# Kernel tuning notes

Measured on AMD Instinct MI355X. Metric: run time of the kernel, lower is better.

Reference implementation:

```python
import math
import jax, jax.numpy as jnp
import numpy as np

B, IMG, CIN = 32, 32, 4
PATCH, HIDDEN, DEPTH, HEADS, MLP = 2, 768, 12, 12, 3072
FREQ, NUM_CLASSES = 256, 1000
GRID = IMG // PATCH
N = GRID * GRID
OUT = PATCH * PATCH * CIN


def _pos_embed(dim, length):
    # faithful port of get_2d_sincos_pos_embed
    g = int(math.sqrt(length))
    grid = np.stack(np.meshgrid(np.arange(g, dtype=np.float32),
                                np.arange(g, dtype=np.float32), indexing='ij')).reshape(2, -1)
    def emb1d(d, pos):
        omega = 1.0 / 10000.0 ** (np.arange(d // 2, dtype=np.float32) / (d / 2.0))
        out = np.einsum('m,d->md', pos, omega)
        return np.concatenate([np.sin(out), np.cos(out)], axis=1)
    pe = np.concatenate([emb1d(dim // 2, grid[0]), emb1d(dim // 2, grid[1])], axis=1)
    return jnp.asarray(pe[None], dtype=jnp.float32)  # [1, N, dim]


def _ln(x):
    # LayerNorm(elementwise_affine=False), eps=1e-5, biased variance
    m = jnp.mean(x, axis=-1, keepdims=True)
    v = jnp.var(x, axis=-1, keepdims=True)
    return (x - m) * jax.lax.rsqrt(v + 1e-5)


def setup_inputs() -> dict:
    key = jax.random.key(0)
    ks = jax.random.split(key, 20)
    w = lambda k, shape: jax.random.normal(k, shape, jnp.float32) * 0.02
    z = lambda *shape: jnp.zeros(shape, jnp.float32)
    return {
        'x': jax.random.normal(ks[0], (B, IMG, IMG, CIN), jnp.float32),
        't': jax.random.uniform(ks[1], (B,), jnp.float32) * 1000.0,
        'y': jax.random.randint(ks[2], (B,), 0, NUM_CLASSES + 1),
        'patch_w': w(ks[3], (PATCH * PATCH * CIN, HIDDEN)), 'patch_b': z(HIDDEN),
        't_w1': w(ks[4], (FREQ, HIDDEN)), 't_b1': z(HIDDEN),
        't_w2': w(ks[5], (HIDDEN, HIDDEN)), 't_b2': z(HIDDEN),
        'label_emb': w(ks[6], (NUM_CLASSES + 1, HIDDEN)),
        'ada_w': w(ks[7], (DEPTH, HIDDEN, 6 * HIDDEN)), 'ada_b': z(DEPTH, 6 * HIDDEN),
        'q_w': w(ks[8], (DEPTH, HIDDEN, HIDDEN)), 'q_b': z(DEPTH, HIDDEN),
        'k_w': w(ks[9], (DEPTH, HIDDEN, HIDDEN)), 'k_b': z(DEPTH, HIDDEN),
        'v_w': w(ks[10], (DEPTH, HIDDEN, HIDDEN)), 'v_b': z(DEPTH, HIDDEN),
        'o_w': w(ks[11], (DEPTH, HIDDEN, HIDDEN)), 'o_b': z(DEPTH, HIDDEN),
        'fc1_w': w(ks[12], (DEPTH, HIDDEN, MLP)), 'fc1_b': z(DEPTH, MLP),
        'fc2_w': w(ks[13], (DEPTH, MLP, HIDDEN)), 'fc2_b': z(DEPTH, HIDDEN),
        'fin_ada_w': w(ks[14], (HIDDEN, 2 * HIDDEN)), 'fin_ada_b': z(2 * HIDDEN),
        'fin_w': w(ks[15], (HIDDEN, OUT)), 'fin_b': z(OUT),
    }


def reference(x, t, y, patch_w, patch_b, t_w1, t_b1, t_w2, t_b2, label_emb,
              ada_w, ada_b, q_w, q_b, k_w, k_b, v_w, v_b, o_w, o_b,
              fc1_w, fc1_b, fc2_w, fc2_b, fin_ada_w, fin_ada_b, fin_w, fin_b):
    Bx = x.shape[0]
    dh = HIDDEN // HEADS
    # patch embed (conv k=p, stride=p == per-patch linear)
    patches = x.reshape(Bx, GRID, PATCH, GRID, PATCH, CIN)
    patches = patches.transpose(0, 1, 3, 2, 4, 5).reshape(Bx, N, PATCH * PATCH * CIN)
    h = patches @ patch_w + patch_b + _pos_embed(HIDDEN, N)
    # timestep embedding: [cos, sin] order
    half = FREQ // 2
    freqs = jnp.exp(-math.log(10000.0) * jnp.arange(half, dtype=jnp.float32) / half)
    args = t.astype(jnp.float32)[:, None] * freqs[None]
    temb = jnp.concatenate([jnp.cos(args), jnp.sin(args)], axis=-1)
    temb = jax.nn.silu(temb @ t_w1 + t_b1) @ t_w2 + t_b2
    c_act = jax.nn.silu(temb + label_emb[y])  # silu applied inside each block on c

    def block(hx, p):
        aw, ab, qw, qb, kw, kb, vw, vb, ow, ob, f1w, f1b, f2w, f2b = p
        ada = c_act @ aw + ab
        sh_m, sc_m, g_m, sh_p, sc_p, g_p = jnp.split(ada, 6, axis=-1)
        xn = _ln(hx) * (1.0 + sc_m[:, None]) + sh_m[:, None]
        q = ((xn @ qw + qb).reshape(Bx, N, HEADS, dh)) / math.sqrt(3.0)
        k = (xn @ kw + kb).reshape(Bx, N, HEADS, dh)
        v = (xn @ vw + vb).reshape(Bx, N, HEADS, dh)
        attn = jax.nn.softmax(jnp.einsum('bqhc,bkhc->bhqk', q, k).astype(jnp.float32), axis=-1)
        yv = jnp.einsum('bhqk,bkhc->bqhc', attn, v).reshape(Bx, N, HIDDEN)
        hx = hx + g_m[:, None] * (yv @ ow + ob)
        xn2 = _ln(hx) * (1.0 + sc_p[:, None]) + sh_p[:, None]
        mlp = jax.nn.gelu(xn2 @ f1w + f1b, approximate=False) @ f2w + f2b
        hx = hx + g_p[:, None] * mlp
        return hx, None

    h, _ = jax.lax.scan(block, h, (ada_w, ada_b, q_w, q_b, k_w, k_b, v_w, v_b,
                                   o_w, o_b, fc1_w, fc1_b, fc2_w, fc2_b))
    # final layer
    fada = c_act @ fin_ada_w + fin_ada_b
    sh, sc = jnp.split(fada, 2, axis=-1)
    out = (_ln(h) * (1.0 + sc[:, None]) + sh[:, None]) @ fin_w + fin_b
    return out  # [B, N, patch*patch*out_channels]
```

## Files before the change

kernel.cpp:

```cpp
#include <hip/hip_runtime.h>
#include <hip/hip_bf16.h>


typedef short  s16x8 __attribute__((ext_vector_type(8)));
typedef float  f32x4 __attribute__((ext_vector_type(4)));

__device__ __forceinline__ float bf2f(unsigned short u) {
    union { unsigned int i; float f; } v; v.i = ((unsigned int)u) << 16; return v.f;
}
__device__ __forceinline__ unsigned short f2bf(float f) {
    union { float f; unsigned int i; } v; v.f = f;
    unsigned int r = (v.i + 0x7FFFu + ((v.i >> 16) & 1u)) >> 16;
    return (unsigned short)r;
}
__device__ __forceinline__ float silu(float v) { return v / (1.f + __expf(-v)); }

__device__ __forceinline__ void gload16(const void* gptr, void* lptr) {
    __builtin_amdgcn_global_load_lds(
        (const __attribute__((address_space(1))) unsigned int*)gptr,
        (__attribute__((address_space(3))) unsigned int*)lptr,
        16, 0, 0);
}

#define ROWS 8192
#define HID  768
#define MLPD 3072
#define ADA_LD 4608

__global__ __launch_bounds__(256) void ada_init(const float* __restrict__ ada_b,
                                                const float* __restrict__ fada_b,
                                                const float* __restrict__ t_b1,
                                                const float* __restrict__ t_b2,
                                                const float* __restrict__ lemb,
                                                const int* __restrict__ y,
                                                float* __restrict__ ada_all,
                                                float* __restrict__ fada,
                                                float* __restrict__ z1,
                                                float* __restrict__ z2)
{
    const int bid = blockIdx.x, tid = threadIdx.x;
    if (bid >= 222) {
        const int col = (bid - 222) * 256 + tid;
        const float b1v = t_b1[col], b2v = t_b2[col];
        for (int r = 0; r < 32; ++r) {
            z1[(size_t)r * HID + col] = b1v;
            z2[(size_t)r * HID + col] = b2v + lemb[(size_t)y[r] * HID + col];
        }
        return;
    }
    const float* Bv; float* Out; int ldw, colb;
    if (bid < 216) {
        const int l = bid / 18; colb = (bid % 18) * 256;
        Bv = ada_b + (size_t)l * ADA_LD; Out = ada_all + (size_t)l * 32 * ADA_LD; ldw = ADA_LD;
    } else {
        colb = (bid - 216) * 256;
        Bv = fada_b; Out = fada; ldw = 1536;
    }
    const int col = colb + tid;
    const float bb = Bv[col];
    #pragma unroll
    for (int r = 0; r < 32; ++r) Out[(size_t)r * ldw + col] = bb;
}

__global__ __launch_bounds__(256) void temb1_k(const float* __restrict__ t,
                                               const float* __restrict__ w1,
                                               float* __restrict__ z1)
{
    __shared__ float tin[128];
    const int b = blockIdx.x, cc = blockIdx.y, kc = blockIdx.z, tid = threadIdx.x;
    const int k0 = kc * 128;
    if (tid < 128) {
        const int k = k0 + tid, j = k & 127;
        const float fr = __expf((float)j * (-9.210340371976184f / 128.f));
        const float a = t[b] * fr;
        tin[tid] = (k < 128) ? cosf(a) : sinf(a);
    }
    __syncthreads();
    const int col = cc * 256 + tid;
    float acc = 0.f;
    #pragma unroll 8
    for (int kk = 0; kk < 128; ++kk) acc += tin[kk] * w1[(size_t)(k0 + kk) * HID + col];
    atomicAdd(&z1[(size_t)b * HID + col], acc);
}

__global__ __launch_bounds__(256) void temb2_k(const float* __restrict__ z1,
                                               const float* __restrict__ w2,
                                               float* __restrict__ z2)
{
    __shared__ float tin[192];
    const int b = blockIdx.x, cc = blockIdx.y, kc = blockIdx.z, tid = threadIdx.x;
    const int k0 = kc * 192;
    if (tid < 192) tin[tid] = silu(z1[(size_t)b * HID + k0 + tid]);
    __syncthreads();
    const int col = cc * 256 + tid;
    float acc = 0.f;
    #pragma unroll 8
    for (int kk = 0; kk < 192; ++kk) acc += tin[kk] * w2[(size_t)(k0 + kk) * HID + col];
    atomicAdd(&z2[(size_t)b * HID + col], acc);
}

__global__ __launch_bounds__(64) void ada_gemm2(const float* __restrict__ z2,
                                                const float* __restrict__ ada_w,
                                                const float* __restrict__ fada_w,
                                                float* __restrict__ ada_all,
                                                float* __restrict__ fada)
{
    const int bx = blockIdx.x, kc = blockIdx.y, tid = threadIdx.x;
    const float* W; float* Out; int ldw, colb;
    if (bx < 216) {
        const int l = bx / 18; colb = (bx % 18) * 256;
        W = ada_w + (size_t)l * HID * ADA_LD; Out = ada_all + (size_t)l * 32 * ADA_LD; ldw = ADA_LD;
    } else {
        colb = (bx - 216) * 256;
        W = fada_w; Out = fada; ldw = 1536;
    }
    const int k0 = kc * 96;
    __shared__ float cs_[32][96];
    for (int i = tid; i < 32 * 96; i += 64)
        cs_[i / 96][i % 96] = silu(z2[(size_t)(i / 96) * HID + k0 + (i % 96)]);
    __syncthreads();
    float acc[4][32];
    #pragma unroll
    for (int j = 0; j < 4; ++j)
        #pragma unroll
        for (int r = 0; r < 32; ++r) acc[j][r] = 0.f;
    #pragma unroll 1
    for (int kk = 0; kk < 96; kk += 4) {
        float wv[4][4];
        #pragma unroll
        for (int i = 0; i < 4; ++i) {
            const float* Wr = W + (size_t)(k0 + kk + i) * ldw + colb + tid;
            #pragma unroll
            for (int j = 0; j < 4; ++j) wv[j][i] = Wr[64 * j];
        }
        #pragma unroll
        for (int r = 0; r < 32; ++r) {
            const float4 cv = *(const float4*)&cs_[r][kk];
            #pragma unroll
            for (int j = 0; j < 4; ++j)
                acc[j][r] += cv.x * wv[j][0] + cv.y * wv[j][1] + cv.z * wv[j][2] + cv.w * wv[j][3];
        }
    }
    #pragma unroll
    for (int j = 0; j < 4; ++j)
        #pragma unroll
        for (int r = 0; r < 32; ++r)
            atomicAdd(&Out[(size_t)r * ldw + colb + tid + 64 * j], acc[j][r]);
}

__global__ __launch_bounds__(256) void patch_embed(const float* __restrict__ x,
                                                   const float* __restrict__ pw,
                                                   const float* __restrict__ pb,
                                                   float* __restrict__ h)
{
    const int row = blockIdx.x;
    const int b = row >> 8, n = row & 255;
    const int gi = n >> 4, gj = n & 15;
    const int tid = threadIdx.x;
    __shared__ float pv[16];
    if (tid < 16) {
        const int pr = tid >> 3, pc = (tid >> 2) & 1, ci = tid & 3;
        pv[tid] = x[((size_t)(b * 32 + gi * 2 + pr) * 32 + (gj * 2 + pc)) * 4 + ci];
    }
    __syncthreads();
    #pragma unroll
    for (int cc = 0; cc < 3; ++cc) {
        const int col = cc * 256 + tid;
        float acc = pb[col];
        #pragma unroll
        for (int i = 0; i < 16; ++i) acc += pv[i] * pw[(size_t)i * HID + col];
        const int d4 = (col < 384) ? col : col - 384;
        const int pos = (col < 384) ? gi : gj;
        const float kf = (float)(d4 < 192 ? d4 : d4 - 192);
        const float om = __expf(kf * (-9.210340371976184f / 192.f));
        const float a = (float)pos * om;
        acc += (d4 < 192) ? sinf(a) : cosf(a);
        h[(size_t)row * HID + col] = acc;
    }
}

__global__ __launch_bounds__(256) void convert_weights(
    const float* __restrict__ q_w, const float* __restrict__ k_w,
    const float* __restrict__ v_w, const float* __restrict__ o_w,
    const float* __restrict__ fc1_w, const float* __restrict__ fc2_w,
    const float* __restrict__ q_b, const float* __restrict__ k_b,
    const float* __restrict__ v_b,
    unsigned short* __restrict__ wbase, size_t slot_stride,
    float* __restrict__ cbias, int first_layer)
{
    const int bid = blockIdx.x;
    const int l = first_layer + bid / 6913;
    const int t = bid % 6913;
    unsigned short* dst = wbase + (size_t)(bid / 6913) * slot_stride;
    const int tid = threadIdx.x;
    if (t == 6912) {
        float* cb = cbias + (size_t)l * 2304;
        for (int i = tid; i < 2304; i += 256) {
            float v;
            if (i < 768)       v = q_b[(size_t)l * 768 + i];
            else if (i < 1536) v = k_b[(size_t)l * 768 + i - 768];
            else               v = v_b[(size_t)l * 768 + i - 1536];
            cb[i] = v;
        }
        return;
    }
    const float* src; int srcN; unsigned short* d; int dLd; int tr, tc;
    if (t < 2304) {
        const int mat = t / 576, tt = t % 576; tr = tt / 24; tc = tt % 24;
        srcN = 768; dLd = 768;
        if (mat == 0)      { src = q_w + (size_t)l * 589824; d = dst; }
        else if (mat == 1) { src = k_w + (size_t)l * 589824; d = dst + 589824; }
        else if (mat == 2) { src = v_w + (size_t)l * 589824; d = dst + 1179648; }
        else               { src = o_w + (size_t)l * 589824; d = dst + 1769472; }
    } else if (t < 4608) {
        const int tt = t - 2304; tr = tt / 96; tc = tt % 96;
        src = fc1_w + (size_t)l * 2359296; srcN = 3072; dLd = 768; d = dst + 2359296;
    } else {
        const int tt = t - 4608; tr = tt / 24; tc = tt % 24;
        src = fc2_w + (size_t)l * 2359296; srcN = 768; dLd = 3072; d = dst + 4718592;
    }
    __shared__ float lt[32][33];
    const int tx = tid & 31, ty = tid >> 5;
    const int r0 = tr * 32, c0 = tc * 32;
    #pragma unroll
    for (int i = 0; i < 4; ++i)
        lt[ty + i * 8][tx] = src[(size_t)(r0 + ty + i * 8) * srcN + c0 + tx];
    __syncthreads();
    #pragma unroll
    for (int i = 0; i < 4; ++i)
        d[(size_t)(c0 + ty + i * 8) * dLd + r0 + tx] = f2bf(lt[tx][ty + i * 8]);
}

__global__ __launch_bounds__(192) void ln_mod(const float* __restrict__ hbuf,
                                              const float* __restrict__ mod,
                                              int sh_off, int sc_off, int mld,
                                              unsigned short* __restrict__ xout)
{
    const int row = blockIdx.x, tid = threadIdx.x;
    const float4 xv = *(const float4*)&hbuf[(size_t)row * HID + tid * 4];
    float s = (xv.x + xv.y) + (xv.z + xv.w);
    float ss = (xv.x * xv.x + xv.y * xv.y) + (xv.z * xv.z + xv.w * xv.w);
    #pragma unroll
    for (int d = 1; d < 64; d <<= 1) { s += __shfl_xor(s, d); ss += __shfl_xor(ss, d); }
    __shared__ float sb[3], ssb[3];
    if ((tid & 63) == 0) { sb[tid >> 6] = s; ssb[tid >> 6] = ss; }
    __syncthreads();
    s = sb[0] + sb[1] + sb[2];
    ss = ssb[0] + ssb[1] + ssb[2];
    const float mean = s * (1.f / 768.f);
    const float var = ss * (1.f / 768.f) - mean * mean;
    const float rs = rsqrtf(var + 1e-5f);
    const int b = row >> 8;
    const float* mrow = mod + (size_t)b * mld;
    const float4 sc = *(const float4*)&mrow[sc_off + tid * 4];
    const float4 sh = *(const float4*)&mrow[sh_off + tid * 4];
    ushort4 o;
    o.x = f2bf((xv.x - mean) * rs * (1.f + sc.x) + sh.x);
    o.y = f2bf((xv.y - mean) * rs * (1.f + sc.y) + sh.y);
    o.z = f2bf((xv.z - mean) * rs * (1.f + sc.z) + sh.z);
    o.w = f2bf((xv.w - mean) * rs * (1.f + sc.w) + sh.w);
    *(ushort4*)&xout[(size_t)row * HID + tid * 4] = o;
}

template<int EPI, int BN>
__global__ __launch_bounds__(256) void gemm_bt(const unsigned short* __restrict__ A,
                                               const unsigned short* __restrict__ Bt,
                                               const float* __restrict__ bias,
                                               void* __restrict__ outp,
                                               const float* __restrict__ gate,
                                               int K, int ldo)
{
    constexpr int BELEMS = BN * 32;
    constexpr int NJ = BN / 32;
    __shared__ unsigned short sAB[2][4096 + BELEMS];
    const int tid = threadIdx.x;
    const int lane = tid & 63;
    const int w = tid >> 6;
    const int wm = w >> 1, wn = w & 1;
    const int rowbase = blockIdx.y << 7;
    const int colbase = blockIdx.x * BN;
    const size_t a0 = (size_t)(rowbase +      (tid >> 2)) * K + (tid & 3) * 8;
    const size_t a1 = (size_t)(rowbase + 64 + (tid >> 2)) * K + (tid & 3) * 8;
    const size_t b0 = (size_t)(colbase +      (tid >> 2)) * K + (tid & 3) * 8;
    size_t b1 = 0;
    if constexpr (BN == 128)
        b1 = (size_t)(colbase + 64 + (tid >> 2)) * K + (tid & 3) * 8;
    const int ldsw = w * 512;
    f32x4 acc[4][NJ];
    #pragma unroll
    for (int i = 0; i < 4; ++i)
        #pragma unroll
        for (int j = 0; j < NJ; ++j) acc[i][j] = (f32x4){0.f, 0.f, 0.f, 0.f};
    const int nk = K >> 5;
    const int lm = lane & 15, lg = lane >> 4;
    {
        unsigned short* base = &sAB[0][0];
        gload16(A + a0,  base + ldsw);
        gload16(A + a1,  base + 2048 + ldsw);
        gload16(Bt + b0, base + 4096 + ldsw);
        if constexpr (BN == 128) gload16(Bt + b1, base + 6144 + ldsw);
    }
    __syncthreads();
    int cur = 0;
    for (int kt = 0; kt < nk; ++kt) {
        if (kt + 1 < nk) {
            const int k0 = (kt + 1) << 5;
            unsigned short* base = &sAB[cur ^ 1][0];
            gload16(A + a0 + k0,  base + ldsw);
            gload16(A + a1 + k0,  base + 2048 + ldsw);
            gload16(Bt + b0 + k0, base + 4096 + ldsw);
            if constexpr (BN == 128) gload16(Bt + b1 + k0, base + 6144 + ldsw);
        }
        const unsigned short* sAc = &sAB[cur][0];
        const unsigned short* sBc = &sAB[cur][4096];
        s16x8 af[4], bfr[NJ];
        #pragma unroll
        for (int mi = 0; mi < 4; ++mi)
            af[mi] = *(const s16x8*)&sAc[(wm * 64 + mi * 16 + lm) * 32 + lg * 8];
        #pragma unroll
        for (int nj = 0; nj < NJ; ++nj)
            bfr[nj] = *(const s16x8*)&sBc[(wn * (16 * NJ) + nj * 16 + lm) * 32 + lg * 8];
        #pragma unroll
        for (int mi = 0; mi < 4; ++mi)
            #pragma unroll
            for (int nj = 0; nj < NJ; ++nj)
                acc[mi][nj] = __builtin_amdgcn_mfma_f32_16x16x32_bf16(af[mi], bfr[nj], acc[mi][nj], 0, 0, 0);
        __syncthreads();
        cur ^= 1;
    }
    float bv[NJ], gv[NJ];
    #pragma unroll
    for (int nj = 0; nj < NJ; ++nj) {
        const int col = colbase + wn * (16 * NJ) + nj * 16 + lm;
        bv[nj] = bias[col];
        if constexpr (EPI == 2) gv[nj] = gate[(size_t)(rowbase >> 8) * ADA_LD + col];
    }
    #pragma unroll
    for (int mi = 0; mi < 4; ++mi) {
        const int row = rowbase + wm * 64 + mi * 16 + (lg << 2);
        #pragma unroll
        for (int nj = 0; nj < NJ; ++nj) {
            const int col = colbase + wn * (16 * NJ) + nj * 16 + lm;
            #pragma unroll
            for (int r = 0; r < 4; ++r) {
                const float v = acc[mi][nj][r] + bv[nj];
                if constexpr (EPI == 0) {
                    ((unsigned short*)outp)[(size_t)(row + r) * ldo + col] = f2bf(v);
                } else if constexpr (EPI == 1) {
                    const float g = 0.5f * v * (1.f + erff(v * 0.70710678118654752f));
                    ((unsigned short*)outp)[(size_t)(row + r) * ldo + col] = f2bf(g);
                } else {
                    float* O = (float*)outp;
                    const size_t idx = (size_t)(row + r) * ldo + col;
                    O[idx] = O[idx] + gv[nj] * v;
                }
            }
        }
    }
}

__global__ __launch_bounds__(256) void attn_fused(const unsigned short* __restrict__ qkv,
                                                  unsigned short* __restrict__ yv)
{
    __shared__ unsigned short Vt[64][264];
    __shared__ unsigned short Psm[4][32 * 72];
    __shared__ float Ssc[4][32];
    const int bid = blockIdx.x;
    const int b = bid / 24, rem = bid % 24, h = rem >> 1, half = rem & 1;
    const int tid = threadIdx.x, w = tid >> 6, lane = tid & 63;
    {
        const int dhg = tid & 7, tk = tid >> 3;
        #pragma unroll
        for (int g = 0; g < 8; ++g) {
            const int tok = tk + g * 32;
            s16x8 vv = *(const s16x8*)(qkv + (size_t)(b * 256 + tok) * 2304 + 1536 + h * 64 + dhg * 8);
            #pragma unroll
            for (int j = 0; j < 8; ++j) Vt[dhg * 8 + j][tok] = (unsigned short)vv[j];
        }
    }
    __syncthreads();
    const int q0 = half * 128 + w * 32;
    const int lm = lane & 15, lg = lane >> 4;
    const unsigned short* Qb = qkv + (size_t)(b * 256 + q0) * 2304 + h * 64;
    s16x8 qf[2][2];
    #pragma unroll
    for (int ni = 0; ni < 2; ++ni)
        #pragma unroll
        for (int kk = 0; kk < 2; ++kk)
            qf[ni][kk] = *(const s16x8*)(Qb + (size_t)(ni * 16 + lm) * 2304 + kk * 32 + lg * 8);
    f32x4 o_[2][4];
    #pragma unroll
    for (int i = 0; i < 2; ++i)
        #pragma unroll
        for (int j = 0; j < 4; ++j) o_[i][j] = (f32x4){0.f, 0.f, 0.f, 0.f};
    float m_[2], l_[2];
    #pragma unroll
    for (int i = 0; i < 2; ++i) { m_[i] = -1e30f; l_[i] = 0.f; }
    const float s3 = 0.57735026918962576f;
    for (int c = 0; c < 4; ++c) {
        f32x4 st[4][2];
        #pragma unroll
        for (int i = 0; i < 4; ++i)
            #pragma unroll
            for (int j = 0; j < 2; ++j) st[i][j] = (f32x4){0.f, 0.f, 0.f, 0.f};
        const unsigned short* Kb = qkv + (size_t)(b * 256 + c * 64) * 2304 + 768 + h * 64;
        __builtin_amdgcn_s_setprio(1);
        #pragma unroll
        for (int kk = 0; kk < 2; ++kk)
            #pragma unroll
            for (int mi = 0; mi < 4; ++mi) {
                const s16x8 kf = *(const s16x8*)(Kb + (size_t)(mi * 16 + lm) * 2304 + kk * 32 + lg * 8);
                #pragma unroll
                for (int ni = 0; ni < 2; ++ni)
                    st[mi][ni] = __builtin_amdgcn_mfma_f32_16x16x32_bf16(kf, qf[ni][kk], st[mi][ni], 0, 0, 0);
            }
        __builtin_amdgcn_s_setprio(0);
        #pragma unroll
        for (int ni = 0; ni < 2; ++ni) {
            float cm = -1e30f;
            #pragma unroll
            for (int mi = 0; mi < 4; ++mi)
                #pragma unroll
                for (int r = 0; r < 4; ++r) cm = fmaxf(cm, st[mi][ni][r]);
            cm = fmaxf(cm, __shfl_xor(cm, 16));
            cm = fmaxf(cm, __shfl_xor(cm, 32));
            cm *= s3;
            const float mn = fmaxf(m_[ni], cm);
            const float corr = __expf(m_[ni] - mn);
            float cs = 0.f;
            #pragma unroll
            for (int mi = 0; mi < 4; ++mi) {
                float p0 = __expf(st[mi][ni][0] * s3 - mn);
                float p1 = __expf(st[mi][ni][1] * s3 - mn);
                float p2 = __expf(st[mi][ni][2] * s3 - mn);
                float p3 = __expf(st[mi][ni][3] * s3 - mn);
                cs += (p0 + p1) + (p2 + p3);
                uint2 pk;
                pk.x = (unsigned int)f2bf(p0) | ((unsigned int)f2bf(p1) << 16);
                pk.y = (unsigned int)f2bf(p2) | ((unsigned int)f2bf(p3) << 16);
                *(uint2*)&Psm[w][(ni * 16 + lm) * 72 + mi * 16 + lg * 4] = pk;
            }
            cs += __shfl_xor(cs, 16);
            cs += __shfl_xor(cs, 32);
            l_[ni] = l_[ni] * corr + cs;
            m_[ni] = mn;
            if (lane < 16) Ssc[w][ni * 16 + lane] = corr;
        }
        asm volatile("" ::: "memory");
        #pragma unroll
        for (int qi = 0; qi < 2; ++qi) {
            float fr[4];
            #pragma unroll
            for (int r = 0; r < 4; ++r) fr[r] = Ssc[w][qi * 16 + lg * 4 + r];
            #pragma unroll
            for (int di = 0; di < 4; ++di)
                #pragma unroll
                for (int r = 0; r < 4; ++r) o_[qi][di][r] *= fr[r];
        }
        __builtin_amdgcn_s_setprio(1);
        #pragma unroll
        for (int kk = 0; kk < 2; ++kk)
            #pragma unroll
            for (int qi = 0; qi < 2; ++qi) {
                const s16x8 pa = *(const s16x8*)&Psm[w][(qi * 16 + lm) * 72 + kk * 32 + lg * 8];
                #pragma unroll
                for (int di = 0; di < 4; ++di) {
                    const s16x8 vb = *(const s16x8*)&Vt[di * 16 + lm][c * 64 + kk * 32 + lg * 8];
                    o_[qi][di] = __builtin_amdgcn_mfma_f32_16x16x32_bf16(pa, vb, o_[qi][di], 0, 0, 0);
                }
            }
        __builtin_amdgcn_s_setprio(0);
    }
    asm volatile("" ::: "memory");
    if (lane < 16) {
        #pragma unroll
        for (int ni = 0; ni < 2; ++ni) Ssc[w][ni * 16 + lane] = 1.f / l_[ni];
    }
    asm volatile("" ::: "memory");
    #pragma unroll
    for (int qi = 0; qi < 2; ++qi) {
        float fr[4];
        #pragma unroll
        for (int r = 0; r < 4; ++r) fr[r] = Ssc[w][qi * 16 + lg * 4 + r];
        #pragma unroll
        for (int di = 0; di < 4; ++di)
            #pragma unroll
            for (int r = 0; r < 4; ++r) {
                const float val = o_[qi][di][r] * fr[r];
                yv[(size_t)(b * 256 + q0 + qi * 16 + lg * 4 + r) * HID + h * 64 + di * 16 + lm] = f2bf(val);
            }
    }
}

__global__ __launch_bounds__(256) void fin_gemm(const unsigned short* __restrict__ xn,
                                                const float* __restrict__ w,
                                                const float* __restrict__ bias,
                                                float* __restrict__ out)
{
    __shared__ unsigned short xs[16 * 768];
    const int rb = blockIdx.x * 16, tid = threadIdx.x;
    #pragma unroll
    for (int i = 0; i < 6; ++i) {
        const int v = tid + i * 256;
        const int row = v / 96, koff = (v % 96) * 8;
        *(s16x8*)&xs[v * 8] = *(const s16x8*)(xn + (size_t)(rb + row) * HID + koff);
    }
    __syncthreads();
    const int r = tid >> 4, o = tid & 15;
    float acc = bias[o];
    #pragma unroll 8
    for (int k = 0; k < 768; ++k) acc += bf2f(xs[r * 768 + k]) * w[(size_t)k * 16 + o];
    out[(size_t)(rb + r) * 16 + o] = acc;
}

extern "C" void kernel_launch(void* const* d_in, const int* in_sizes, int n_in,
                              void* d_out, int out_size, void* d_ws, size_t ws_size,
                              hipStream_t stream)
{
    const float* x        = (const float*)d_in[0];
    const float* t        = (const float*)d_in[1];
    const int*   y        = (const int*)d_in[2];
    const float* patch_w  = (const float*)d_in[3];
    const float* patch_b  = (const float*)d_in[4];
    const float* t_w1     = (const float*)d_in[5];
    const float* t_b1     = (const float*)d_in[6];
    const float* t_w2     = (const float*)d_in[7];
    const float* t_b2     = (const float*)d_in[8];
    const float* label_e  = (const float*)d_in[9];
    const float* ada_w    = (const float*)d_in[10];
    const float* ada_b    = (const float*)d_in[11];
    const float* q_w      = (const float*)d_in[12];
    const float* q_b      = (const float*)d_in[13];
    const float* k_w      = (const float*)d_in[14];
    const float* k_b      = (const float*)d_in[15];
    const float* v_w      = (const float*)d_in[16];
    const float* v_b      = (const float*)d_in[17];
    const float* o_w      = (const float*)d_in[18];
    const float* o_b      = (const float*)d_in[19];
    const float* fc1_w    = (const float*)d_in[20];
    const float* fc1_b    = (const float*)d_in[21];
    const float* fc2_w    = (const float*)d_in[22];
    const float* fc2_b    = (const float*)d_in[23];
    const float* fada_w   = (const float*)d_in[24];
    const float* fada_b   = (const float*)d_in[25];
    const float* fin_w    = (const float*)d_in[26];
    const float* fin_b    = (const float*)d_in[27];

    char* ws = (char*)d_ws;
    size_t off = 0;
    auto alloc = [&](size_t bytes) { size_t o = off; off = (off + bytes + 255) & ~(size_t)255; return o; };
    const size_t OFF_H    = alloc((size_t)ROWS * HID * 4);
    const size_t OFF_XN   = alloc((size_t)ROWS * HID * 2);
    const size_t OFF_QKV  = alloc((size_t)ROWS * 2304 * 2);
    const size_t OFF_YV   = alloc((size_t)ROWS * HID * 2);
    const size_t OFF_MLP  = alloc((size_t)ROWS * MLPD * 2);
    const size_t OFF_ADA  = alloc((size_t)12 * 32 * ADA_LD * 4);
    const size_t OFF_FADA = alloc((size_t)32 * 1536 * 4);
    const size_t OFF_Z2   = alloc((size_t)32 * HID * 4);
    const size_t OFF_Z1   = alloc((size_t)32 * HID * 4);
    const size_t OFF_CB   = alloc((size_t)12 * 2304 * 4);
    const size_t OFF_W    = off;
    const size_t WSLOT_ELEMS = 7077888;
    const bool big = (ws_size >= OFF_W + (size_t)12 * WSLOT_ELEMS * 2);

    float*          h     = (float*)(ws + OFF_H);
    unsigned short* xn    = (unsigned short*)(ws + OFF_XN);
    unsigned short* qkv   = (unsigned short*)(ws + OFF_QKV);
    unsigned short* yv    = (unsigned short*)(ws + OFF_YV);
    unsigned short* mlp   = (unsigned short*)(ws + OFF_MLP);
    float*          adaA  = (float*)(ws + OFF_ADA);
    float*          fada  = (float*)(ws + OFF_FADA);
    float*          z2    = (float*)(ws + OFF_Z2);
    float*          z1    = (float*)(ws + OFF_Z1);
    float*          cbias = (float*)(ws + OFF_CB);
    unsigned short* wsW   = (unsigned short*)(ws + OFF_W);

    ada_init<<<225, 256, 0, stream>>>(ada_b, fada_b, t_b1, t_b2, label_e, y,
                                      adaA, fada, z1, z2);
    temb1_k<<<dim3(32, 3, 2), 256, 0, stream>>>(t, t_w1, z1);
    temb2_k<<<dim3(32, 3, 4), 256, 0, stream>>>(z1, t_w2, z2);
    ada_gemm2<<<dim3(222, 8), 64, 0, stream>>>(z2, ada_w, fada_w, adaA, fada);
    patch_embed<<<8192, 256, 0, stream>>>(x, patch_w, patch_b, h);
    if (big) {
        convert_weights<<<6913 * 12, 256, 0, stream>>>(q_w, k_w, v_w, o_w, fc1_w, fc2_w,
                                                       q_b, k_b, v_b, wsW, WSLOT_ELEMS, cbias, 0);
    }

    for (int l = 0; l < 12; ++l) {
        unsigned short* wslot = wsW + (big ? (size_t)l * WSLOT_ELEMS : 0);
        if (!big) {
            convert_weights<<<6913, 256, 0, stream>>>(q_w, k_w, v_w, o_w, fc1_w, fc2_w,
                                                      q_b, k_b, v_b, wslot, 0, cbias, l);
        }
        unsigned short* qkvT = wslot;
        unsigned short* oT   = wslot + 1769472;
        unsigned short* f1T  = wslot + 2359296;
        unsigned short* f2T  = wslot + 4718592;
        float* ada_l  = adaA + (size_t)l * 32 * ADA_LD;
        float* cb_l   = cbias + (size_t)l * 2304;

        ln_mod<<<8192, 192, 0, stream>>>(h, ada_l, 0, 768, ADA_LD, xn);
        gemm_bt<0, 128><<<dim3(18, 64), 256, 0, stream>>>(xn, qkvT, cb_l, qkv, nullptr, 768, 2304);
        attn_fused<<<768, 256, 0, stream>>>(qkv, yv);
        gemm_bt<2, 64><<<dim3(12, 64), 256, 0, stream>>>(yv, oT, o_b + (size_t)l * 768, h,
                                                         ada_l + 1536, 768, 768);
        ln_mod<<<8192, 192, 0, stream>>>(h, ada_l, 2304, 3072, ADA_LD, xn);
        gemm_bt<1, 128><<<dim3(24, 64), 256, 0, stream>>>(xn, f1T, fc1_b + (size_t)l * 3072, mlp,
                                                          nullptr, 768, 3072);
        gemm_bt<2, 64><<<dim3(12, 64), 256, 0, stream>>>(mlp, f2T, fc2_b + (size_t)l * 768, h,
                                                         ada_l + 3840, 3072, 768);
    }

    ln_mod<<<8192, 192, 0, stream>>>(h, fada, 0, 768, 1536, xn);
    fin_gemm<<<512, 256, 0, stream>>>(xn, fin_w, fin_b, (float*)d_out);
}
```

Baseline: 3.550 ms.

## Add 256x128 triple-buffered MFMA GEMM for QKV and FC1, widen ada_gemm2 blocks

Adds a new bf16 MFMA GEMM kernel with a 256x128 output tile, 8 waves, three LDS stages filled by direct global-to-LDS loads, XOR-swizzled LDS reads, and an interleaved load/compute schedule using barriers and priority hints. It replaces the 128-row GEMM for the QKV projection and the FC1+GELU projection to get more data reuse per block and to hide load latency. Separately, ada_gemm2 now uses 256 threads, each computing one column instead of four, which gives more parallelism but less register reuse. The bigger tile uses a large amount of LDS and registers, which limits occupancy and leaves fewer blocks in the grid.

```diff
diff --git a/kernel.cpp b/kernel.cpp
--- a/kernel.cpp
+++ b/kernel.cpp
@@ -99,11 +99,11 @@
     atomicAdd(&z2[(size_t)b * HID + col], acc);
 }
 
-__global__ __launch_bounds__(64) void ada_gemm2(const float* __restrict__ z2,
-                                                const float* __restrict__ ada_w,
-                                                const float* __restrict__ fada_w,
-                                                float* __restrict__ ada_all,
-                                                float* __restrict__ fada)
+__global__ __launch_bounds__(256) void ada_gemm2(const float* __restrict__ z2,
+                                                 const float* __restrict__ ada_w,
+                                                 const float* __restrict__ fada_w,
+                                                 float* __restrict__ ada_all,
+                                                 float* __restrict__ fada)
 {
     const int bx = blockIdx.x, kc = blockIdx.y, tid = threadIdx.x;
     const float* W; float* Out; int ldw, colb;
@@ -114,38 +114,29 @@
         colb = (bx - 216) * 256;
         W = fada_w; Out = fada; ldw = 1536;
     }
+    const int col = colb + tid;
     const int k0 = kc * 96;
     __shared__ float cs_[32][96];
-    for (int i = tid; i < 32 * 96; i += 64)
+    for (int i = tid; i < 32 * 96; i += 256)
         cs_[i / 96][i % 96] = silu(z2[(size_t)(i / 96) * HID + k0 + (i % 96)]);
     __syncthreads();
-    float acc[4][32];
-    #pragma unroll
-    for (int j = 0; j < 4; ++j)
-        #pragma unroll
-        for (int r = 0; r < 32; ++r) acc[j][r] = 0.f;
-    #pragma unroll 1
+    float acc[32];
+    #pragma unroll
+    for (int r = 0; r < 32; ++r) acc[r] = 0.f;
+    #pragma unroll 2
     for (int kk = 0; kk < 96; kk += 4) {
-        float wv[4][4];
-        #pragma unroll
-        for (int i = 0; i < 4; ++i) {
-            const float* Wr = W + (size_t)(k0 + kk + i) * ldw + colb + tid;
-            #pragma unroll
-            for (int j = 0; j < 4; ++j) wv[j][i] = Wr[64 * j];
-        }
+        const float w0 = W[(size_t)(k0 + kk) * ldw + col];
+        const float w1 = W[(size_t)(k0 + kk + 1) * ldw + col];
+        const float w2 = W[(size_t)(k0 + kk + 2) * ldw + col];
+        const float w3 = W[(size_t)(k0 + kk + 3) * ldw + col];
         #pragma unroll
         for (int r = 0; r < 32; ++r) {
             const float4 cv = *(const float4*)&cs_[r][kk];
-            #pragma unroll
-            for (int j = 0; j < 4; ++j)
-                acc[j][r] += cv.x * wv[j][0] + cv.y * wv[j][1] + cv.z * wv[j][2] + cv.w * wv[j][3];
-        }
-    }
-    #pragma unroll
-    for (int j = 0; j < 4; ++j)
-        #pragma unroll
-        for (int r = 0; r < 32; ++r)
-            atomicAdd(&Out[(size_t)r * ldw + colb + tid + 64 * j], acc[j][r]);
+            acc[r] += cv.x * w0 + cv.y * w1 + cv.z * w2 + cv.w * w3;
+        }
+    }
+    #pragma unroll
+    for (int r = 0; r < 32; ++r) atomicAdd(&Out[(size_t)r * ldw + col], acc[r]);
 }
 
 __global__ __launch_bounds__(256) void patch_embed(const float* __restrict__ x,
@@ -357,6 +348,159 @@
             }
         }
     }
+}
+
+template<int EPI>
+__global__ __launch_bounds__(512) void gemm256(const unsigned short* __restrict__ A,
+                                               const unsigned short* __restrict__ Bt,
+                                               const float* __restrict__ bias,
+                                               unsigned short* __restrict__ outp,
+                                               int K, int ldo)
+{
+    __shared__ char ldsb[3 * 49152];
+    const int tid = threadIdx.x;
+    const int lane = tid & 63, w = tid >> 6;
+    const int wm = w >> 2, wn = w & 3;
+    const int lm = lane & 15, lg = lane >> 4;
+    const int rowT = blockIdx.y << 8;
+    const int colT = blockIdx.x << 7;
+    const int nt = K >> 6;
+    int srow[2], scol[2];
+    #pragma unroll
+    for (int i = 0; i < 2; ++i) {
+        const int L = i * 8192 + tid * 16;
+        const int P = L ^ (((L >> 9) & 3) << 5);
+        srow[i] = P >> 7;
+        scol[i] = (P & 127) >> 1;
+    }
+    const int wub = (w << 10);
+    const int sx = ((lm >> 2) & 3) << 5;
+
+    f32x4 acc[8][2];
+    #pragma unroll
+    for (int i = 0; i < 8; ++i)
+        #pragma unroll
+        for (int j = 0; j < 2; ++j) acc[i][j] = (f32x4){0.f, 0.f, 0.f, 0.f};
+
+    auto stageA = [&](int sb, int kt, int h) {
+        char* dst = ldsb + sb * 49152 + h * 16384 + wub;
+        const size_t kb = (size_t)kt << 6;
+        #pragma unroll
+        for (int i = 0; i < 2; ++i)
+            gload16(A + (size_t)(rowT + h * 128 + srow[i]) * K + kb + scol[i],
+                    dst + i * 8192);
+    };
+    auto stageB = [&](int sb, int kt) {
+        char* dst = ldsb + sb * 49152 + 32768 + wub;
+        const size_t kb = (size_t)kt << 6;
+        #pragma unroll
+        for (int i = 0; i < 2; ++i)
+            gload16(Bt + (size_t)(colT + srow[i]) * K + kb + scol[i],
+                    dst + i * 8192);
+    };
+    #define GBAR() do { asm volatile("" ::: "memory"); __builtin_amdgcn_s_barrier(); asm volatile("" ::: "memory"); } while (0)
+
+    stageA(0, 0, 0); stageA(0, 0, 1); stageB(0, 0);
+    stageA(1, 1, 0); stageA(1, 1, 1); stageB(1, 1);
+    asm volatile("s_waitcnt vmcnt(6)" ::: "memory");
+    GBAR();
+
+    for (int t = 0; t < nt; ++t) {
+        const char* rb = ldsb + (t % 3) * 49152;
+        const char* rbA = rb + wm * 16384;
+        const char* rbB = rb + 32768;
+        const int sb = (t + 2) % 3;
+        const bool st = (t + 2) < nt;
+        s16x8 bf0[2], bf1[2], af[4], af2[4];
+        #pragma unroll
+        for (int nj = 0; nj < 2; ++nj) {
+            const int lc = wn * 32 + nj * 16 + lm;
+            bf0[nj] = *(const s16x8*)(rbB + ((lc * 128 + lg * 16) ^ sx));
+            bf1[nj] = *(const s16x8*)(rbB + ((lc * 128 + 64 + lg * 16) ^ sx));
+        }
+        #pragma unroll
+        for (int mi = 0; mi < 4; ++mi) {
+            const int lr = mi * 16 + lm;
+            af[mi] = *(const s16x8*)(rbA + ((lr * 128 + lg * 16) ^ sx));
+        }
+        if (st) stageA(sb, t + 2, 0);
+        GBAR();
+        __builtin_amdgcn_s_setprio(1);
+        #pragma unroll
+        for (int mi = 0; mi < 4; ++mi)
+            #pragma unroll
+            for (int nj = 0; nj < 2; ++nj)
+                acc[mi][nj] = __builtin_amdgcn_mfma_f32_16x16x32_bf16(af[mi], bf0[nj], acc[mi][nj], 0, 0, 0);
+        __builtin_amdgcn_s_setprio(0);
+        GBAR();
+        #pragma unroll
+        for (int mi = 0; mi < 4; ++mi) {
+            const int lr = mi * 16 + lm;
+            af2[mi] = *(const s16x8*)(rbA + ((lr * 128 + 64 + lg * 16) ^ sx));
+        }
+        if (st) stageA(sb, t + 2, 1);
+        GBAR();
+        __builtin_amdgcn_s_setprio(1);
+        #pragma unroll
+        for (int mi = 0; mi < 4; ++mi)
+            #pragma unroll
+            for (int nj = 0; nj < 2; ++nj)
+                acc[mi][nj] = __builtin_amdgcn_mfma_f32_16x16x32_bf16(af2[mi], bf1[nj], acc[mi][nj], 0, 0, 0);
+        __builtin_amdgcn_s_setprio(0);
+        GBAR();
+        #pragma unroll
+        for (int mi = 0; mi < 4; ++mi) {
+            const int lr = 64 + mi * 16 + lm;
+            af[mi] = *(const s16x8*)(rbA + ((lr * 128 + lg * 16) ^ sx));
+        }
+        if (st) stageB(sb, t + 2);
+        GBAR();
+        __builtin_amdgcn_s_setprio(1);
+        #pragma unroll
+        for (int mi = 0; mi < 4; ++mi)
+            #pragma unroll
+            for (int nj = 0; nj < 2; ++nj)
+                acc[4 + mi][nj] = __builtin_amdgcn_mfma_f32_16x16x32_bf16(af[mi], bf0[nj], acc[4 + mi][nj], 0, 0, 0);
+        __builtin_amdgcn_s_setprio(0);
+        GBAR();
+        #pragma unroll
+        for (int mi = 0; mi < 4; ++mi) {
+            const int lr = 64 + mi * 16 + lm;
+            af2[mi] = *(const s16x8*)(rbA + ((lr * 128 + 64 + lg * 16) ^ sx));
+        }
+        if (st) asm volatile("s_waitcnt vmcnt(6)" ::: "memory");
+        else    asm volatile("s_waitcnt vmcnt(0)" ::: "memory");
+        GBAR();
+        __builtin_amdgcn_s_setprio(1);
+        #pragma unroll
+        for (int mi = 0; mi < 4; ++mi)
+            #pragma unroll
+            for (int nj = 0; nj < 2; ++nj)
+                acc[4 + mi][nj] = __builtin_amdgcn_mfma_f32_16x16x32_bf16(af2[mi], bf1[nj], acc[4 + mi][nj], 0, 0, 0);
+        __builtin_amdgcn_s_setprio(0);
+        GBAR();
+    }
+    #undef GBAR
+    float bv[2];
+    #pragma unroll
+    for (int nj = 0; nj < 2; ++nj) bv[nj] = bias[colT + wn * 32 + nj * 16 + lm];
+    #pragma unroll
+    for (int mh = 0; mh < 2; ++mh)
+        #pragma unroll
+        for (int mi = 0; mi < 4; ++mi) {
+            const int row = rowT + wm * 128 + mh * 64 + mi * 16 + (lg << 2);
+            #pragma unroll
+            for (int nj = 0; nj < 2; ++nj) {
+                const int col = colT + wn * 32 + nj * 16 + lm;
+                #pragma unroll
+                for (int r = 0; r < 4; ++r) {
+                    float v = acc[mh * 4 + mi][nj][r] + bv[nj];
+                    if constexpr (EPI == 1)
+                        v = 0.5f * v * (1.f + erff(v * 0.70710678118654752f));
+                    outp[(size_t)(row + r) * ldo + col] = f2bf(v);
+                }
+            }
+        }
 }
 
 __global__ __launch_bounds__(256) void attn_fused(const unsigned short* __restrict__ qkv,
@@ -579,7 +723,7 @@
                                       adaA, fada, z1, z2);
     temb1_k<<<dim3(32, 3, 2), 256, 0, stream>>>(t, t_w1, z1);
     temb2_k<<<dim3(32, 3, 4), 256, 0, stream>>>(z1, t_w2, z2);
-    ada_gemm2<<<dim3(222, 8), 64, 0, stream>>>(z2, ada_w, fada_w, adaA, fada);
+    ada_gemm2<<<dim3(222, 8), 256, 0, stream>>>(z2, ada_w, fada_w, adaA, fada);
     patch_embed<<<8192, 256, 0, stream>>>(x, patch_w, patch_b, h);
     if (big) {
         convert_weights<<<6913 * 12, 256, 0, stream>>>(q_w, k_w, v_w, o_w, fc1_w, fc2_w,
@@ -600,13 +744,12 @@
         float* cb_l   = cbias + (size_t)l * 2304;
 
         ln_mod<<<8192, 192, 0, stream>>>(h, ada_l, 0, 768, ADA_LD, xn);
-        gemm_bt<0, 128><<<dim3(18, 64), 256, 0, stream>>>(xn, qkvT, cb_l, qkv, nullptr, 768, 2304);
+        gemm256<0><<<dim3(18, 32), 512, 0, stream>>>(xn, qkvT, cb_l, qkv, 768, 2304);
         attn_fused<<<768, 256, 0, stream>>>(qkv, yv);
         gemm_bt<2, 64><<<dim3(12, 64), 256, 0, stream>>>(yv, oT, o_b + (size_t)l * 768, h,
                                                          ada_l + 1536, 768, 768);
         ln_mod<<<8192, 192, 0, stream>>>(h, ada_l, 2304, 3072, ADA_LD, xn);
-        gemm_bt<1, 128><<<dim3(24, 64), 256, 0, stream>>>(xn, f1T, fc1_b + (size_t)l * 3072, mlp,
-                                                          nullptr, 768, 3072);
+        gemm256<1><<<dim3(24, 32), 512, 0, stream>>>(xn, f1T, fc1_b + (size_t)l * 3072, mlp, 768, 3072);
         gemm_bt<2, 64><<<dim3(12, 64), 256, 0, stream>>>(mlp, f2T, fc2_b + (size_t)l * 768, h,
                                                          ada_l + 3840, 3072, 768);
     }
```

Result: slower. 3.767 ms (+6.1%).
